# Kernel optimization log

Measured on AMD Instinct MI355X. Metric: run time of the kernel, lower is better.

The kernel has to match this reference:

```python
import jax, jax.numpy as jnp
import numpy as np

N_NODES = 50000
N_EDGES = 150000
N_GRAPHS = 1024
IN_DIM = 78
OUT_DIM = 64
HEADS = 10
HID = OUT_DIM * HEADS  # 640
NEG_SLOPE = 0.2


def _add_self_loops(edge_index, num_nodes):
    loop = jnp.arange(num_nodes, dtype=edge_index.dtype)
    src = jnp.concatenate([edge_index[0], loop])
    dst = jnp.concatenate([edge_index[1], loop])
    return src, dst


def gatv2_conv(x, edge_index, Wl, Wr, att, bias, heads, out_dim):
    # PyG GATv2Conv (share_weights=False, concat=True, add_self_loops=True),
    # inference mode so attention dropout is a no-op.
    N = x.shape[0]
    src, dst = _add_self_loops(edge_index, N)
    xl = (x @ Wl).reshape(N, heads, out_dim)  # source transform
    xr = (x @ Wr).reshape(N, heads, out_dim)  # target transform
    s = jax.nn.leaky_relu(xl[src] + xr[dst], NEG_SLOPE)      # [E,H,C]
    logits = jnp.einsum('ehc,hc->eh', s, att)                # [E,H]
    m = jax.ops.segment_max(logits, dst, num_segments=N)     # [N,H] (self-loops => no empty segs)
    ex = jnp.exp(logits - m[dst])
    den = jax.ops.segment_sum(ex, dst, num_segments=N)
    alpha = ex / den[dst]                                    # scatter-softmax over in-edges
    out = jax.ops.segment_sum(alpha[:, :, None] * xl[src], dst, num_segments=N)
    return out.reshape(N, heads * out_dim) + bias


def gcn_conv(x, edge_index, W, b):
    N = x.shape[0]
    src, dst = _add_self_loops(edge_index, N)
    deg = jax.ops.segment_sum(jnp.ones(src.shape[0], x.dtype), dst, num_segments=N)
    dinv = jax.lax.rsqrt(jnp.maximum(deg, 1.0))
    norm = dinv[src] * dinv[dst]                             # [E]
    xw = x @ W
    return jax.ops.segment_sum(norm[:, None] * xw[src], dst, num_segments=N) + b


def setup_inputs() -> dict:
    key = jax.random.key(0)
    ks = jax.random.split(key, 16)
    x = jax.random.normal(ks[0], (N_NODES, IN_DIM), dtype=jnp.float32)
    edge_index = jax.random.randint(ks[1], (2, N_EDGES), 0, N_NODES, dtype=jnp.int64)
    batch = jnp.sort(jax.random.randint(ks[2], (N_NODES,), 0, N_GRAPHS, dtype=jnp.int64))

    def glorot(k, shape, fan_in):
        return jax.random.normal(k, shape, dtype=jnp.float32) * (1.0 / np.sqrt(fan_in))

    return {
        'x': x, 'edge_index': edge_index, 'batch': batch,
        'Wl1': glorot(ks[3], (IN_DIM, HID), IN_DIM),
        'Wr1': glorot(ks[4], (IN_DIM, HID), IN_DIM),
        'a1': glorot(ks[5], (HEADS, OUT_DIM), OUT_DIM),
        'b1': jnp.zeros((HID,), jnp.float32),
        'Wl2': glorot(ks[6], (HID, HID), HID),
        'Wr2': glorot(ks[7], (HID, HID), HID),
        'a2': glorot(ks[8], (1, HID), HID),
        'b2': jnp.zeros((HID,), jnp.float32),
        'Wg': glorot(ks[9], (HID, HID), HID),
        'bg': jnp.zeros((HID,), jnp.float32),
    }


def reference(x, edge_index, batch, Wl1, Wr1, a1, b1, Wl2, Wr2, a2, b2, Wg, bg):
    # inference: feature dropout layers are identity
    h = jax.nn.elu(gatv2_conv(x, edge_index, Wl1, Wr1, a1, b1, HEADS, OUT_DIM))
    h = gatv2_conv(h, edge_index, Wl2, Wr2, a2, b2, 1, HID)
    h = gcn_conv(h, edge_index, Wg, bg)
    h = jax.nn.relu(h)
    # global max pool + global mean pool per graph
    gmax = jax.ops.segment_max(h, batch, num_segments=N_GRAPHS)
    cnt = jax.ops.segment_sum(jnp.ones((h.shape[0],), h.dtype), batch, num_segments=N_GRAPHS)
    gmean = jax.ops.segment_sum(h, batch, num_segments=N_GRAPHS) / jnp.maximum(cnt, 1.0)[:, None]
    return jnp.concatenate([gmax, gmean], axis=1)
```

## Files before the change

kernel.cpp:

```cpp
#include <hip/hip_runtime.h>
#include <hip/hip_bf16.h>
#include <cstdint>
#include <cstddef>

typedef __hip_bfloat16 bf16;

#define N_NODES  50000
#define N_EDGES  150000
#define E_TOT    (N_EDGES + N_NODES)
#define N_TILES  ((E_TOT + 15) / 16)
#define N_GRAPHS 1024
#define IN_DIM   78
#define K1P      128
#define OUT_DIM  64
#define HEADS    10
#define HID      640
#define NEG_SLOPE 0.2f
#define SCB      ((N_NODES + 255) / 256)

static __device__ __forceinline__ float b2f(bf16 v){ return __bfloat162float(v); }
static __device__ __forceinline__ bf16  f2b(float v){ return __float2bfloat16(v); }

__device__ __forceinline__ int clampi(int v, int hi){ return v < 0 ? 0 : (v >= hi ? hi - 1 : v); }

__device__ __forceinline__ float bf2f_bits(short s){
  return __uint_as_float(((unsigned)(unsigned short)s) << 16);
}
__device__ __forceinline__ short f2bf_bits(float v){
  unsigned u = __float_as_uint(v);
  return (short)((u + 0x7fffu + ((u >> 16) & 1u)) >> 16);
}
__device__ __forceinline__ short f2bf_trunc(float v){
  return (short)(__float_as_uint(v) >> 16);
}

__global__ __launch_bounds__(256) void fill_u32(unsigned* __restrict__ p, unsigned v, int n){
  int i = blockIdx.x * 256 + threadIdx.x;
  if (i < n) p[i] = v;
}

__global__ __launch_bounds__(256) void conv_x(const float* __restrict__ x, bf16* __restrict__ XB){
  int i = blockIdx.x * 256 + threadIdx.x;
  if (i >= N_NODES * K1P) return;
  int n = i / K1P, k = i - n * K1P;
  XB[i] = f2b(k < IN_DIM ? x[(size_t)n * IN_DIM + k] : 0.f);
}

__global__ __launch_bounds__(256) void conv_wT2(const float* __restrict__ W0,
                                                const float* __restrict__ W1,
                                                bf16* __restrict__ WT,
                                                int K, int N, int Kp){
  int i = blockIdx.x * 256 + threadIdx.x;
  const int per = N * Kp;
  if (i >= 2 * per) return;
  int m = i / per, r = i - m * per;
  const float* W = m == 0 ? W0 : W1;
  int n = r / Kp, k = r - n * Kp;
  WT[i] = f2b(k < K ? W[(size_t)k * N + n] : 0.f);
}

__global__ __launch_bounds__(256) void conv_wT3t(const float* __restrict__ W0,
                                                 const float* __restrict__ W1,
                                                 const float* __restrict__ W2,
                                                 bf16* __restrict__ WT){
  __shared__ float t[32][33];
  int m = blockIdx.z;
  const float* W = m == 0 ? W0 : (m == 1 ? W1 : W2);
  int n0 = blockIdx.x * 32, k0 = blockIdx.y * 32;
  int tx = threadIdx.x & 31, ty = threadIdx.x >> 5;
#pragma unroll
  for (int r = 0; r < 32; r += 8)
    t[ty + r][tx] = W[(size_t)(k0 + ty + r) * HID + n0 + tx];
  __syncthreads();
  bf16* O = WT + (size_t)m * HID * HID;
#pragma unroll
  for (int r = 0; r < 32; r += 8)
    O[(size_t)(n0 + ty + r) * HID + k0 + tx] = f2b(t[tx][ty + r]);
}

__global__ __launch_bounds__(256) void conv_attP(const float* __restrict__ a, bf16* __restrict__ P,
                                                 int heads){
  int i = blockIdx.x * 256 + threadIdx.x;
  if (i >= (HID / 32) * 512) return;
  int chunk = i >> 9;
  int lane  = (i >> 3) & 63;
  int j     = i & 7;
  int h = lane & 15;
  int k = (lane >> 4) * 8 + j;
  int c = chunk * 32 + k;
  float v = 0.f;
  if (heads == HEADS){ if (h < HEADS && (c >> 6) == h) v = a[c]; }
  else               { if (h == 0) v = a[c]; }
  P[i] = f2b(v);
}

#define BM 128
#define BN 128
#define BK 64

typedef __attribute__((ext_vector_type(8))) short bf16x8;
typedef __attribute__((ext_vector_type(4))) float f32x4;

typedef const __attribute__((address_space(1))) unsigned gu32;
typedef __attribute__((address_space(3))) unsigned lu32;

__global__ __launch_bounds__(256) void mfma_gemm(const bf16* __restrict__ A,
                                                 const bf16* __restrict__ BT,
                                                 bf16* __restrict__ C0,
                                                 bf16* __restrict__ C1,
                                                 int M, int Kp, int NB){
  int d   = blockIdx.x;
  int xcd = d & 7, j = d >> 3;
  int cb  = j % NB, ri = j / NB;
  int rb  = ri * 8 + xcd;
  const int row0 = rb * BM;
  if (row0 >= M) return;
  const int col0 = cb * BN;

  __shared__ short As[BM * BK];
  __shared__ short Bs[BN * BK];
  const int tid  = threadIdx.x;
  const int lane = tid & 63;
  const int wave = tid >> 6;
  const int wr   = (wave >> 1) * 64;
  const int wc   = (wave & 1) * 64;
  const int l15  = lane & 15;
  const int quad = lane >> 4;
  const int sw   = l15 & 7;

  const bf16* aptr[4];
  const bf16* bptr[4];
  lu32* lda[4];
  lu32* ldb[4];
#pragma unroll
  for (int t = 0; t < 4; ++t){
    int ci = (t * 4 + wave) * 64 + lane;
    int r  = ci >> 3;
    int sc = (ci & 7) ^ (r & 7);
    int gr = row0 + r; if (gr >= M) gr = M - 1;
    aptr[t] = A  + (size_t)gr * Kp + sc * 8;
    bptr[t] = BT + (size_t)(col0 + r) * Kp + sc * 8;
    lda[t]  = (lu32*)(&As[(t * 4 + wave) * 512]);
    ldb[t]  = (lu32*)(&Bs[(t * 4 + wave) * 512]);
  }

  f32x4 acc[4][4];
#pragma unroll
  for (int i = 0; i < 4; ++i)
#pragma unroll
    for (int jj = 0; jj < 4; ++jj) acc[i][jj] = (f32x4){0.f, 0.f, 0.f, 0.f};

  for (int k0 = 0; k0 < Kp; k0 += BK){
#pragma unroll
    for (int t = 0; t < 4; ++t){
      __builtin_amdgcn_global_load_lds((gu32*)(aptr[t] + k0), lda[t], 16, 0, 0);
      __builtin_amdgcn_global_load_lds((gu32*)(bptr[t] + k0), ldb[t], 16, 0, 0);
    }
    __syncthreads();

#pragma unroll
    for (int ks = 0; ks < 2; ++ks){
      const int slotA = ((ks * 4 + quad) ^ sw) * 8;
      bf16x8 af[4], bfr[4];
#pragma unroll
      for (int i = 0; i < 4; ++i)
        af[i] = *(bf16x8*)(&As[(wr + i * 16 + l15) * BK + slotA]);
#pragma unroll
      for (int jj = 0; jj < 4; ++jj)
        bfr[jj] = *(bf16x8*)(&Bs[(wc + jj * 16 + l15) * BK + slotA]);
#pragma unroll
      for (int i = 0; i < 4; ++i)
#pragma unroll
        for (int jj = 0; jj < 4; ++jj)
          acc[i][jj] = __builtin_amdgcn_mfma_f32_16x16x32_bf16(af[i], bfr[jj], acc[i][jj], 0, 0, 0);
    }
    __syncthreads();
  }

  if (row0 + BM <= M){
#pragma unroll
    for (int i = 0; i < 4; ++i){
#pragma unroll
      for (int jj = 0; jj < 4; ++jj){
        int gc = col0 + wc + jj * 16 + l15;
        bf16* Cp = (gc < HID) ? C0 : C1;
        size_t cc = (gc < HID) ? gc : gc - HID;
        size_t base = (size_t)(row0 + wr + i * 16 + quad * 4) * HID + cc;
#pragma unroll
        for (int r = 0; r < 4; ++r)
          Cp[base + (size_t)r * HID] = f2b(acc[i][jj][r]);
      }
    }
  } else {
#pragma unroll
    for (int i = 0; i < 4; ++i){
#pragma unroll
      for (int jj = 0; jj < 4; ++jj){
        int gc = col0 + wc + jj * 16 + l15;
        bf16* Cp = (gc < HID) ? C0 : C1;
        int cc   = (gc < HID) ? gc : gc - HID;
#pragma unroll
        for (int r = 0; r < 4; ++r){
          int gr = row0 + wr + i * 16 + quad * 4 + r;
          if (gr < M) Cp[(size_t)gr * HID + cc] = f2b(acc[i][jj][r]);
        }
      }
    }
  }
}

__global__ __launch_bounds__(256) void count_deg(const int* __restrict__ edst, int* __restrict__ degi){
  int e = blockIdx.x * 256 + threadIdx.x;
  if (e >= N_EDGES) return;
  atomicAdd(&degi[clampi(edst[e], N_NODES)], 1);
}

__global__ __launch_bounds__(256) void scan_blk(const int* __restrict__ degi,
                                                int* __restrict__ rowp,
                                                float* __restrict__ dinv,
                                                int* __restrict__ bsum){
  __shared__ int wsum[4];
  int b = blockIdx.x, tid = threadIdx.x;
  int i = b * 256 + tid;
  int lane = tid & 63, wv = tid >> 6;
  int v = (i < N_NODES) ? degi[i] : 0;
  int incl = v;
#pragma unroll
  for (int ofs = 1; ofs < 64; ofs <<= 1){
    int t = __shfl_up(incl, ofs);
    if (lane >= ofs) incl += t;
  }
  if (lane == 63) wsum[wv] = incl;
  __syncthreads();
  int woff = 0;
#pragma unroll
  for (int w = 0; w < 4; ++w) if (w < wv) woff += wsum[w];
  if (i < N_NODES){
    rowp[i] = woff + incl - v;
    dinv[i] = rsqrtf((float)(v + 1));
  }
  if (tid == 0) bsum[b] = wsum[0] + wsum[1] + wsum[2] + wsum[3];
}

__global__ __launch_bounds__(256) void scan_top(int* __restrict__ bsum, int* __restrict__ rowp){
  __shared__ int wsum[4];
  int tid = threadIdx.x, lane = tid & 63, wv = tid >> 6;
  int v = (tid < SCB) ? bsum[tid] : 0;
  int incl = v;
#pragma unroll
  for (int ofs = 1; ofs < 64; ofs <<= 1){
    int t = __shfl_up(incl, ofs);
    if (lane >= ofs) incl += t;
  }
  if (lane == 63) wsum[wv] = incl;
  __syncthreads();
  int woff = 0;
#pragma unroll
  for (int w = 0; w < 4; ++w) if (w < wv) woff += wsum[w];
  if (tid < SCB) bsum[tid] = woff + incl - v;
  if (tid == 255) rowp[N_NODES] = woff + incl;
}

__global__ __launch_bounds__(256) void scan_add(const int* __restrict__ bsum,
                                                int* __restrict__ rowp,
                                                int* __restrict__ curs){
  int i = blockIdx.x * 256 + threadIdx.x;
  if (i >= N_NODES) return;
  int r = rowp[i] + bsum[blockIdx.x];
  rowp[i] = r; curs[i] = r;
}

__global__ __launch_bounds__(256) void bucket_edges(const int* __restrict__ esrc,
                                                    const int* __restrict__ edst,
                                                    int* __restrict__ curs,
                                                    int* __restrict__ srcg,
                                                    int* __restrict__ dstg){
  int e = blockIdx.x * 256 + threadIdx.x;
  if (e >= N_EDGES) return;
  int d = clampi(edst[e], N_NODES);
  int pos = atomicAdd(&curs[d], 1);
  srcg[pos] = clampi(esrc[e], N_NODES);
  dstg[pos] = d;
}

__global__ __launch_bounds__(256) void logits_mfma(const bf16* __restrict__ xl,
                                                   const bf16* __restrict__ xr,
                                                   const int* __restrict__ srcg,
                                                   const int* __restrict__ dstg,
                                                   const bf16* __restrict__ attP,
                                                   float* __restrict__ LOG,
                                                   int only0){
  int wid  = (blockIdx.x * 256 + threadIdx.x) >> 6;
  int lane = threadIdx.x & 63;
  if (wid >= N_TILES) return;
  const int l15 = lane & 15, quad = lane >> 4;
  int p = wid * 16 + l15; if (p >= E_TOT) p = E_TOT - 1;
  int s, d;
  if (p < N_EDGES){ s = srcg[p]; d = dstg[p]; }
  else            { s = d = p - N_EDGES; }
  const bf16* ps = xl + (size_t)s * HID + quad * 8;
  const bf16* pd = xr + (size_t)d * HID + quad * 8;
  const bf16* pw = attP + lane * 8;

  f32x4 acc = (f32x4){0.f, 0.f, 0.f, 0.f};
  for (int k0 = 0; k0 < HID; k0 += 64){
    bf16x8 va0 = *(const bf16x8*)(ps + k0);
    bf16x8 vb0 = *(const bf16x8*)(pd + k0);
    bf16x8 va1 = *(const bf16x8*)(ps + k0 + 32);
    bf16x8 vb1 = *(const bf16x8*)(pd + k0 + 32);
    bf16x8 t0, t1;
#pragma unroll
    for (int j = 0; j < 8; ++j){
      float v0 = bf2f_bits(va0[j]) + bf2f_bits(vb0[j]);
      v0 *= (v0 > 0.f) ? 1.f : NEG_SLOPE;
      t0[j] = f2bf_trunc(v0);
      float v1 = bf2f_bits(va1[j]) + bf2f_bits(vb1[j]);
      v1 *= (v1 > 0.f) ? 1.f : NEG_SLOPE;
      t1[j] = f2bf_trunc(v1);
    }
    bf16x8 wb0 = *(const bf16x8*)(pw + (k0 >> 5) * 512);
    bf16x8 wb1 = *(const bf16x8*)(pw + ((k0 >> 5) + 1) * 512);
    acc = __builtin_amdgcn_mfma_f32_16x16x32_bf16(t0, wb0, acc, 0, 0, 0);
    acc = __builtin_amdgcn_mfma_f32_16x16x32_bf16(t1, wb1, acc, 0, 0, 0);
  }
  int er = wid * 16 + quad * 4;
  if (only0){
    if (l15 == 0){
#pragma unroll
      for (int r = 0; r < 4; ++r){
        int ee = er + r;
        if (ee < E_TOT) LOG[ee] = acc[r];
      }
    }
  } else {
#pragma unroll
    for (int r = 0; r < 4; ++r){
      int ee = er + r;
      if (ee < E_TOT) LOG[(size_t)ee * 16 + l15] = acc[r];
    }
  }
}

__global__ __launch_bounds__(256) void gat1_agg(const bf16* __restrict__ xl,
                                                const int* __restrict__ srcg,
                                                const int* __restrict__ rowp,
                                                const float* __restrict__ LOG,
                                                const float* __restrict__ bias,
                                                bf16* __restrict__ H){
  int n    = (blockIdx.x * 256 + threadIdx.x) >> 6;
  int lane = threadIdx.x & 63;
  if (n >= N_NODES) return;
  const int l15 = lane & 15;
  const int hA = lane >> 3;
  const int hB = 8 + (lane >> 5);
  int r0 = rowp[n], r1 = rowp[n + 1];

  float lself = LOG[(size_t)(N_EDGES + n) * 16 + l15];
  float m = lself;
  for (int p = r0; p < r1; ++p) m = fmaxf(m, LOG[(size_t)p * 16 + l15]);

  float p0  = __expf(lself - m);
  float den = p0;
  float accA[8], accB[2];
  {
    float pA = __shfl(p0, hA), pB = __shfl(p0, hB);
    const bf16* xn = xl + (size_t)n * HID;
    bf16x8 va = *(const bf16x8*)(xn + 8 * lane);
    unsigned vb = *(const unsigned*)(xn + 512 + 2 * lane);
#pragma unroll
    for (int j = 0; j < 8; ++j) accA[j] = pA * bf2f_bits(va[j]);
    accB[0] = pB * bf2f_bits((short)(vb & 0xffff));
    accB[1] = pB * bf2f_bits((short)(vb >> 16));
  }
  int p = r0;
  for (; p + 1 < r1; p += 2){
    int s0 = srcg[p], s1 = srcg[p + 1];
    float l0 = LOG[(size_t)p * 16 + l15];
    float l1 = LOG[(size_t)(p + 1) * 16 + l15];
    const bf16* xs0 = xl + (size_t)s0 * HID;
    const bf16* xs1 = xl + (size_t)s1 * HID;
    bf16x8 va0 = *(const bf16x8*)(xs0 + 8 * lane);
    bf16x8 va1 = *(const bf16x8*)(xs1 + 8 * lane);
    unsigned vb0 = *(const unsigned*)(xs0 + 512 + 2 * lane);
    unsigned vb1 = *(const unsigned*)(xs1 + 512 + 2 * lane);
    float pv0 = __expf(l0 - m), pv1 = __expf(l1 - m);
    den += pv0 + pv1;
    float pA0 = __shfl(pv0, hA), pB0 = __shfl(pv0, hB);
    float pA1 = __shfl(pv1, hA), pB1 = __shfl(pv1, hB);
#pragma unroll
    for (int j = 0; j < 8; ++j) accA[j] += pA0 * bf2f_bits(va0[j]) + pA1 * bf2f_bits(va1[j]);
    accB[0] += pB0 * bf2f_bits((short)(vb0 & 0xffff)) + pB1 * bf2f_bits((short)(vb1 & 0xffff));
    accB[1] += pB0 * bf2f_bits((short)(vb0 >> 16))    + pB1 * bf2f_bits((short)(vb1 >> 16));
  }
  if (p < r1){
    int s = srcg[p];
    float pv = __expf(LOG[(size_t)p * 16 + l15] - m);
    den += pv;
    float pA = __shfl(pv, hA), pB = __shfl(pv, hB);
    const bf16* xs = xl + (size_t)s * HID;
    bf16x8 va = *(const bf16x8*)(xs + 8 * lane);
    unsigned vb = *(const unsigned*)(xs + 512 + 2 * lane);
#pragma unroll
    for (int j = 0; j < 8; ++j) accA[j] += pA * bf2f_bits(va[j]);
    accB[0] += pB * bf2f_bits((short)(vb & 0xffff));
    accB[1] += pB * bf2f_bits((short)(vb >> 16));
  }
  float dA = __shfl(den, hA), dB = __shfl(den, hB);
  float4 bA0 = *(const float4*)(bias + 8 * lane);
  float4 bA1 = *(const float4*)(bias + 8 * lane + 4);
  float2 bB  = *(const float2*)(bias + 512 + 2 * lane);
  bf16x8 oA;
  float bAa[8] = {bA0.x, bA0.y, bA0.z, bA0.w, bA1.x, bA1.y, bA1.z, bA1.w};
#pragma unroll
  for (int j = 0; j < 8; ++j){
    float v = accA[j] / dA + bAa[j];
    v = v > 0.f ? v : (__expf(v) - 1.f);
    oA[j] = f2bf_bits(v);
  }
  float v0 = accB[0] / dB + bB.x; v0 = v0 > 0.f ? v0 : (__expf(v0) - 1.f);
  float v1 = accB[1] / dB + bB.y; v1 = v1 > 0.f ? v1 : (__expf(v1) - 1.f);
  bf16* hn = H + (size_t)n * HID;
  *(bf16x8*)(hn + 8 * lane) = oA;
  unsigned ob = (unsigned)(unsigned short)f2bf_bits(v0) |
                ((unsigned)(unsigned short)f2bf_bits(v1) << 16);
  *(unsigned*)(hn + 512 + 2 * lane) = ob;
}

__global__ __launch_bounds__(256) void gat2_agg(const bf16* __restrict__ xl,
                                                const int* __restrict__ srcg,
                                                const int* __restrict__ rowp,
                                                const float* __restrict__ LOG,
                                                const float* __restrict__ bias,
                                                bf16* __restrict__ H){
  int n    = (blockIdx.x * 256 + threadIdx.x) >> 6;
  int lane = threadIdx.x & 63;
  if (n >= N_NODES) return;
  int r0 = rowp[n], r1 = rowp[n + 1];

  float lself = LOG[N_EDGES + n];
  float m = lself;
  for (int p = r0; p < r1; ++p) m = fmaxf(m, LOG[p]);

  float p0  = __expf(lself - m);
  float den = p0;
  float accA[8], accB[2];
  {
    const bf16* xn = xl + (size_t)n * HID;
    bf16x8 va = *(const bf16x8*)(xn + 8 * lane);
    unsigned vb = *(const unsigned*)(xn + 512 + 2 * lane);
#pragma unroll
    for (int j = 0; j < 8; ++j) accA[j] = p0 * bf2f_bits(va[j]);
    accB[0] = p0 * bf2f_bits((short)(vb & 0xffff));
    accB[1] = p0 * bf2f_bits((short)(vb >> 16));
  }
  int p = r0;
  for (; p + 1 < r1; p += 2){
    int s0 = srcg[p], s1 = srcg[p + 1];
    float pv0 = __expf(LOG[p] - m), pv1 = __expf(LOG[p + 1] - m);
    const bf16* xs0 = xl + (size_t)s0 * HID;
    const bf16* xs1 = xl + (size_t)s1 * HID;
    bf16x8 va0 = *(const bf16x8*)(xs0 + 8 * lane);
    bf16x8 va1 = *(const bf16x8*)(xs1 + 8 * lane);
    unsigned vb0 = *(const unsigned*)(xs0 + 512 + 2 * lane);
    unsigned vb1 = *(const unsigned*)(xs1 + 512 + 2 * lane);
    den += pv0 + pv1;
#pragma unroll
    for (int j = 0; j < 8; ++j) accA[j] += pv0 * bf2f_bits(va0[j]) + pv1 * bf2f_bits(va1[j]);
    accB[0] += pv0 * bf2f_bits((short)(vb0 & 0xffff)) + pv1 * bf2f_bits((short)(vb1 & 0xffff));
    accB[1] += pv0 * bf2f_bits((short)(vb0 >> 16))    + pv1 * bf2f_bits((short)(vb1 >> 16));
  }
  if (p < r1){
    int s = srcg[p];
    float pv = __expf(LOG[p] - m);
    den += pv;
    const bf16* xs = xl + (size_t)s * HID;
    bf16x8 va = *(const bf16x8*)(xs + 8 * lane);
    unsigned vb = *(const unsigned*)(xs + 512 + 2 * lane);
#pragma unroll
    for (int j = 0; j < 8; ++j) accA[j] += pv * bf2f_bits(va[j]);
    accB[0] += pv * bf2f_bits((short)(vb & 0xffff));
    accB[1] += pv * bf2f_bits((short)(vb >> 16));
  }
  float inv = 1.f / den;
  float4 bA0 = *(const float4*)(bias + 8 * lane);
  float4 bA1 = *(const float4*)(bias + 8 * lane + 4);
  float2 bB  = *(const float2*)(bias + 512 + 2 * lane);
  float bAa[8] = {bA0.x, bA0.y, bA0.z, bA0.w, bA1.x, bA1.y, bA1.z, bA1.w};
  bf16x8 oA;
#pragma unroll
  for (int j = 0; j < 8; ++j) oA[j] = f2bf_bits(accA[j] * inv + bAa[j]);
  bf16* hn = H + (size_t)n * HID;
  *(bf16x8*)(hn + 8 * lane) = oA;
  unsigned ob = (unsigned)(unsigned short)f2bf_bits(accB[0] * inv + bB.x) |
                ((unsigned)(unsigned short)f2bf_bits(accB[1] * inv + bB.y) << 16);
  *(unsigned*)(hn + 512 + 2 * lane) = ob;
}

__global__ __launch_bounds__(256) void gcn_gather(const bf16* __restrict__ xw,
                                                  const int* __restrict__ srcg,
                                                  const int* __restrict__ rowp,
                                                  const float* __restrict__ dinv,
                                                  const float* __restrict__ bg,
                                                  bf16* __restrict__ h3){
  int n    = (blockIdx.x * 256 + threadIdx.x) >> 6;
  int lane = threadIdx.x & 63;
  if (n >= N_NODES) return;
  int r0 = rowp[n], r1 = rowp[n + 1];

  float dn = dinv[n];
  float accA[8], accB[2];
  {
    float w = dn * dn;
    const bf16* xn = xw + (size_t)n * HID;
    bf16x8 va = *(const bf16x8*)(xn + 8 * lane);
    unsigned vb = *(const unsigned*)(xn + 512 + 2 * lane);
#pragma unroll
    for (int j = 0; j < 8; ++j) accA[j] = w * bf2f_bits(va[j]);
    accB[0] = w * bf2f_bits((short)(vb & 0xffff));
    accB[1] = w * bf2f_bits((short)(vb >> 16));
  }
  int p = r0;
  for (; p + 1 < r1; p += 2){
    int s0 = srcg[p], s1 = srcg[p + 1];
    float w0 = dinv[s0] * dn, w1 = dinv[s1] * dn;
    const bf16* xs0 = xw + (size_t)s0 * HID;
    const bf16* xs1 = xw + (size_t)s1 * HID;
    bf16x8 va0 = *(const bf16x8*)(xs0 + 8 * lane);
    bf16x8 va1 = *(const bf16x8*)(xs1 + 8 * lane);
    unsigned vb0 = *(const unsigned*)(xs0 + 512 + 2 * lane);
    unsigned vb1 = *(const unsigned*)(xs1 + 512 + 2 * lane);
#pragma unroll
    for (int j = 0; j < 8; ++j) accA[j] += w0 * bf2f_bits(va0[j]) + w1 * bf2f_bits(va1[j]);
    accB[0] += w0 * bf2f_bits((short)(vb0 & 0xffff)) + w1 * bf2f_bits((short)(vb1 & 0xffff));
    accB[1] += w0 * bf2f_bits((short)(vb0 >> 16))    + w1 * bf2f_bits((short)(vb1 >> 16));
  }
  if (p < r1){
    int s = srcg[p];
    float w = dinv[s] * dn;
    const bf16* xs = xw + (size_t)s * HID;
    bf16x8 va = *(const bf16x8*)(xs + 8 * lane);
    unsigned vb = *(const unsigned*)(xs + 512 + 2 * lane);
#pragma unroll
    for (int j = 0; j < 8; ++j) accA[j] += w * bf2f_bits(va[j]);
    accB[0] += w * bf2f_bits((short)(vb & 0xffff));
    accB[1] += w * bf2f_bits((short)(vb >> 16));
  }
  float4 bA0 = *(const float4*)(bg + 8 * lane);
  float4 bA1 = *(const float4*)(bg + 8 * lane + 4);
  float2 bB  = *(const float2*)(bg + 512 + 2 * lane);
  float bAa[8] = {bA0.x, bA0.y, bA0.z, bA0.w, bA1.x, bA1.y, bA1.z, bA1.w};
  bf16x8 oA;
#pragma unroll
  for (int j = 0; j < 8; ++j) oA[j] = f2bf_bits(fmaxf(accA[j] + bAa[j], 0.f));
  bf16* hn = h3 + (size_t)n * HID;
  *(bf16x8*)(hn + 8 * lane) = oA;
  unsigned ob = (unsigned)(unsigned short)f2bf_bits(fmaxf(accB[0] + bB.x, 0.f)) |
                ((unsigned)(unsigned short)f2bf_bits(fmaxf(accB[1] + bB.y, 0.f)) << 16);
  *(unsigned*)(hn + 512 + 2 * lane) = ob;
}

__global__ __launch_bounds__(256) void graph_bounds(const int* __restrict__ batch,
                                                    int* __restrict__ gstart){
  int n = blockIdx.x * 256 + threadIdx.x;
  if (n >= N_NODES) return;
  int b = clampi(batch[n], N_GRAPHS);
  if (n == 0){
    for (int g = 0; g <= b; ++g) gstart[g] = 0;
  } else {
    int bp = clampi(batch[n - 1], N_GRAPHS);
    for (int g = bp + 1; g <= b; ++g) gstart[g] = n;
  }
  if (n == N_NODES - 1){
    for (int g = b + 1; g <= N_GRAPHS; ++g) gstart[g] = N_NODES;
  }
}

__global__ __launch_bounds__(640) void pool_graph(const bf16* __restrict__ h3,
                                                  const int* __restrict__ gstart,
                                                  float* __restrict__ out){
  int g = blockIdx.x;
  int c = threadIdx.x;
  int n0 = gstart[g], n1 = gstart[g + 1];
  float mx = 0.f, sm = 0.f;
  for (int n = n0; n < n1; ++n){
    float v = b2f(h3[(size_t)n * HID + c]);
    mx = fmaxf(mx, v); sm += v;
  }
  float mean = (n1 > n0) ? sm / (float)(n1 - n0) : 0.f;
  out[(size_t)g * 2 * HID + c]       = mx;
  out[(size_t)g * 2 * HID + HID + c] = mean;
}

extern "C" void kernel_launch(void* const* d_in, const int* in_sizes, int n_in,
                              void* d_out, int out_size, void* d_ws, size_t ws_size,
                              hipStream_t stream){
  const float* x     = (const float*)d_in[0];
  const int*   ei    = (const int*)d_in[1];
  const int*   batch = (const int*)d_in[2];
  const float* Wl1 = (const float*)d_in[3];
  const float* Wr1 = (const float*)d_in[4];
  const float* a1  = (const float*)d_in[5];
  const float* b1  = (const float*)d_in[6];
  const float* Wl2 = (const float*)d_in[7];
  const float* Wr2 = (const float*)d_in[8];
  const float* a2  = (const float*)d_in[9];
  const float* b2  = (const float*)d_in[10];
  const float* Wg  = (const float*)d_in[11];
  const float* bg  = (const float*)d_in[12];
  const int* esrc = ei;
  const int* edst = ei + N_EDGES;

  char* ws = (char*)d_ws;
  size_t off = 0;
  auto take = [&](size_t bytes)->char*{
    char* p = ws + off; off = (off + bytes + 255) & ~(size_t)255; return p;
  };
  bf16*     X1   = (bf16*)    take((size_t)N_NODES * HID * 2);
  bf16*     X2   = (bf16*)    take((size_t)N_NODES * HID * 2);
  bf16*     H    = (bf16*)    take((size_t)N_NODES * HID * 2);
  bf16*     XB   = (bf16*)    take((size_t)N_NODES * K1P * 2);
  bf16*     WT1l = (bf16*)    take((size_t)HID * K1P * 2);
  bf16*     WT1r = (bf16*)    take((size_t)HID * K1P * 2);
  bf16*     WT2l = (bf16*)    take((size_t)HID * HID * 2);
  bf16*     WT2r = (bf16*)    take((size_t)HID * HID * 2);
  bf16*     WTg  = (bf16*)    take((size_t)HID * HID * 2);
  bf16*     AT1P = (bf16*)    take((size_t)(HID / 32) * 512 * 2);
  bf16*     AT2P = (bf16*)    take((size_t)(HID / 32) * 512 * 2);
  float*    LOG  = (float*)   take((size_t)E_TOT * 16 * 4);
  int*      DEGI = (int*)     take((size_t)N_NODES * 4);
  int*      ROWP = (int*)     take((size_t)(N_NODES + 1) * 4);
  int*      CURS = (int*)     take((size_t)N_NODES * 4);
  int*      SRCG = (int*)     take((size_t)N_EDGES * 4);
  int*      DSTG = (int*)     take((size_t)N_EDGES * 4);
  float*    DINV = (float*)   take((size_t)N_NODES * 4);
  int*      GST  = (int*)     take((size_t)(N_GRAPHS + 1) * 4);
  int*      BSUM = (int*)     take((size_t)SCB * 4);

  dim3 blk(256);
  auto fill = [&](void* p, unsigned v, int n){
    fill_u32<<<dim3((n + 255) / 256), blk, 0, stream>>>((unsigned*)p, v, n);
  };
  const int MB8     = ((N_NODES + BM - 1) / BM + 7) / 8;
  const int nblocks = (N_NODES * 64 + 255) / 256;
  const int lblocks = (N_TILES * 64 + 255) / 256;
  const int reblk   = (N_EDGES + 255) / 256;
  const int apn     = (HID / 32) * 512;

  conv_x<<<(N_NODES * K1P + 255) / 256, blk, 0, stream>>>(x, XB);
  conv_wT2<<<(2 * HID * K1P + 255) / 256, blk, 0, stream>>>(Wl1, Wr1, WT1l, IN_DIM, HID, K1P);
  conv_wT3t<<<dim3(HID / 32, HID / 32, 3), blk, 0, stream>>>(Wl2, Wr2, Wg, WT2l);
  conv_attP<<<(apn + 255) / 256, blk, 0, stream>>>(a1, AT1P, HEADS);
  conv_attP<<<(apn + 255) / 256, blk, 0, stream>>>(a2, AT2P, 1);
  fill(DEGI, 0u, N_NODES);
  count_deg<<<reblk, blk, 0, stream>>>(edst, DEGI);
  scan_blk<<<dim3(SCB), blk, 0, stream>>>(DEGI, ROWP, DINV, BSUM);
  scan_top<<<dim3(1), blk, 0, stream>>>(BSUM, ROWP);
  scan_add<<<dim3(SCB), blk, 0, stream>>>(BSUM, ROWP, CURS);
  bucket_edges<<<reblk, blk, 0, stream>>>(esrc, edst, CURS, SRCG, DSTG);
  graph_bounds<<<(N_NODES + 255) / 256, blk, 0, stream>>>(batch, GST);

  mfma_gemm<<<dim3(8 * MB8 * 10), blk, 0, stream>>>(XB, WT1l, X1, X2, N_NODES, K1P, 10);
  logits_mfma<<<lblocks, blk, 0, stream>>>(X1, X2, SRCG, DSTG, AT1P, LOG, 0);
  gat1_agg<<<nblocks, blk, 0, stream>>>(X1, SRCG, ROWP, LOG, b1, H);

  mfma_gemm<<<dim3(8 * MB8 * 10), blk, 0, stream>>>(H, WT2l, X1, X2, N_NODES, HID, 10);
  logits_mfma<<<lblocks, blk, 0, stream>>>(X1, X2, SRCG, DSTG, AT2P, LOG, 1);
  gat2_agg<<<nblocks, blk, 0, stream>>>(X1, SRCG, ROWP, LOG, b2, H);

  mfma_gemm<<<dim3(8 * MB8 * 5), blk, 0, stream>>>(H, WTg, X1, X1, N_NODES, HID, 5);
  gcn_gather<<<nblocks, blk, 0, stream>>>(X1, SRCG, ROWP, DINV, bg, X2);
  pool_graph<<<dim3(N_GRAPHS), dim3(640), 0, stream>>>(X2, GST, (float*)d_out);
}
```

Measured before the change: 611.8 us.

## Fuse GATv2 logit computation into aggregation with online softmax

Removes the separate MFMA logits kernels and the edge-logit buffer, so each node's wavefront computes attention logits on the fly from the gathered source row and its own target row. It uses an online (running-max) softmax so the aggregation needs a single pass over in-edges. This avoids writing and re-reading a per-edge logit array and a second gather of source rows. In exchange it replaces MFMA dot products with scalar FMAs plus cross-lane shuffle reductions, and adds extra exp rescaling per edge pair.

```diff
diff --git a/kernel.cpp b/kernel.cpp
--- a/kernel.cpp
+++ b/kernel.cpp
@@ -7,8 +7,6 @@
 
 #define N_NODES  50000
 #define N_EDGES  150000
-#define E_TOT    (N_EDGES + N_NODES)
-#define N_TILES  ((E_TOT + 15) / 16)
 #define N_GRAPHS 1024
 #define IN_DIM   78
 #define K1P      128
@@ -29,9 +27,6 @@
 __device__ __forceinline__ short f2bf_bits(float v){
   unsigned u = __float_as_uint(v);
   return (short)((u + 0x7fffu + ((u >> 16) & 1u)) >> 16);
-}
-__device__ __forceinline__ short f2bf_trunc(float v){
-  return (short)(__float_as_uint(v) >> 16);
 }
 
 __global__ __launch_bounds__(256) void fill_u32(unsigned* __restrict__ p, unsigned v, int n){
@@ -76,22 +71,6 @@
 #pragma unroll
   for (int r = 0; r < 32; r += 8)
     O[(size_t)(n0 + ty + r) * HID + k0 + tx] = f2b(t[tx][ty + r]);
-}
-
-__global__ __launch_bounds__(256) void conv_attP(const float* __restrict__ a, bf16* __restrict__ P,
-                                                 int heads){
-  int i = blockIdx.x * 256 + threadIdx.x;
-  if (i >= (HID / 32) * 512) return;
-  int chunk = i >> 9;
-  int lane  = (i >> 3) & 63;
-  int j     = i & 7;
-  int h = lane & 15;
-  int k = (lane >> 4) * 8 + j;
-  int c = chunk * 32 + k;
-  float v = 0.f;
-  if (heads == HEADS){ if (h < HEADS && (c >> 6) == h) v = a[c]; }
-  else               { if (h == 0) v = a[c]; }
-  P[i] = f2b(v);
 }
 
 #define BM 128
@@ -283,204 +262,258 @@
   dstg[pos] = d;
 }
 
-__global__ __launch_bounds__(256) void logits_mfma(const bf16* __restrict__ xl,
-                                                   const bf16* __restrict__ xr,
-                                                   const int* __restrict__ srcg,
-                                                   const int* __restrict__ dstg,
-                                                   const bf16* __restrict__ attP,
-                                                   float* __restrict__ LOG,
-                                                   int only0){
-  int wid  = (blockIdx.x * 256 + threadIdx.x) >> 6;
-  int lane = threadIdx.x & 63;
-  if (wid >= N_TILES) return;
-  const int l15 = lane & 15, quad = lane >> 4;
-  int p = wid * 16 + l15; if (p >= E_TOT) p = E_TOT - 1;
-  int s, d;
-  if (p < N_EDGES){ s = srcg[p]; d = dstg[p]; }
-  else            { s = d = p - N_EDGES; }
-  const bf16* ps = xl + (size_t)s * HID + quad * 8;
-  const bf16* pd = xr + (size_t)d * HID + quad * 8;
-  const bf16* pw = attP + lane * 8;
-
-  f32x4 acc = (f32x4){0.f, 0.f, 0.f, 0.f};
-  for (int k0 = 0; k0 < HID; k0 += 64){
-    bf16x8 va0 = *(const bf16x8*)(ps + k0);
-    bf16x8 vb0 = *(const bf16x8*)(pd + k0);
-    bf16x8 va1 = *(const bf16x8*)(ps + k0 + 32);
-    bf16x8 vb1 = *(const bf16x8*)(pd + k0 + 32);
-    bf16x8 t0, t1;
-#pragma unroll
-    for (int j = 0; j < 8; ++j){
-      float v0 = bf2f_bits(va0[j]) + bf2f_bits(vb0[j]);
-      v0 *= (v0 > 0.f) ? 1.f : NEG_SLOPE;
-      t0[j] = f2bf_trunc(v0);
-      float v1 = bf2f_bits(va1[j]) + bf2f_bits(vb1[j]);
-      v1 *= (v1 > 0.f) ? 1.f : NEG_SLOPE;
-      t1[j] = f2bf_trunc(v1);
-    }
-    bf16x8 wb0 = *(const bf16x8*)(pw + (k0 >> 5) * 512);
-    bf16x8 wb1 = *(const bf16x8*)(pw + ((k0 >> 5) + 1) * 512);
-    acc = __builtin_amdgcn_mfma_f32_16x16x32_bf16(t0, wb0, acc, 0, 0, 0);
-    acc = __builtin_amdgcn_mfma_f32_16x16x32_bf16(t1, wb1, acc, 0, 0, 0);
-  }
-  int er = wid * 16 + quad * 4;
-  if (only0){
-    if (l15 == 0){
-#pragma unroll
-      for (int r = 0; r < 4; ++r){
-        int ee = er + r;
-        if (ee < E_TOT) LOG[ee] = acc[r];
-      }
-    }
-  } else {
-#pragma unroll
-    for (int r = 0; r < 4; ++r){
-      int ee = er + r;
-      if (ee < E_TOT) LOG[(size_t)ee * 16 + l15] = acc[r];
-    }
-  }
-}
-
-__global__ __launch_bounds__(256) void gat1_agg(const bf16* __restrict__ xl,
-                                                const int* __restrict__ srcg,
-                                                const int* __restrict__ rowp,
-                                                const float* __restrict__ LOG,
-                                                const float* __restrict__ bias,
-                                                bf16* __restrict__ H){
-  int n    = (blockIdx.x * 256 + threadIdx.x) >> 6;
-  int lane = threadIdx.x & 63;
-  if (n >= N_NODES) return;
-  const int l15 = lane & 15;
-  const int hA = lane >> 3;
-  const int hB = 8 + (lane >> 5);
-  int r0 = rowp[n], r1 = rowp[n + 1];
-
-  float lself = LOG[(size_t)(N_EDGES + n) * 16 + l15];
-  float m = lself;
-  for (int p = r0; p < r1; ++p) m = fmaxf(m, LOG[(size_t)p * 16 + l15]);
-
-  float p0  = __expf(lself - m);
-  float den = p0;
-  float accA[8], accB[2];
-  {
-    float pA = __shfl(p0, hA), pB = __shfl(p0, hB);
-    const bf16* xn = xl + (size_t)n * HID;
-    bf16x8 va = *(const bf16x8*)(xn + 8 * lane);
-    unsigned vb = *(const unsigned*)(xn + 512 + 2 * lane);
-#pragma unroll
-    for (int j = 0; j < 8; ++j) accA[j] = pA * bf2f_bits(va[j]);
-    accB[0] = pB * bf2f_bits((short)(vb & 0xffff));
-    accB[1] = pB * bf2f_bits((short)(vb >> 16));
-  }
-  int p = r0;
-  for (; p + 1 < r1; p += 2){
-    int s0 = srcg[p], s1 = srcg[p + 1];
-    float l0 = LOG[(size_t)p * 16 + l15];
-    float l1 = LOG[(size_t)(p + 1) * 16 + l15];
-    const bf16* xs0 = xl + (size_t)s0 * HID;
-    const bf16* xs1 = xl + (size_t)s1 * HID;
-    bf16x8 va0 = *(const bf16x8*)(xs0 + 8 * lane);
-    bf16x8 va1 = *(const bf16x8*)(xs1 + 8 * lane);
-    unsigned vb0 = *(const unsigned*)(xs0 + 512 + 2 * lane);
-    unsigned vb1 = *(const unsigned*)(xs1 + 512 + 2 * lane);
-    float pv0 = __expf(l0 - m), pv1 = __expf(l1 - m);
-    den += pv0 + pv1;
-    float pA0 = __shfl(pv0, hA), pB0 = __shfl(pv0, hB);
-    float pA1 = __shfl(pv1, hA), pB1 = __shfl(pv1, hB);
-#pragma unroll
-    for (int j = 0; j < 8; ++j) accA[j] += pA0 * bf2f_bits(va0[j]) + pA1 * bf2f_bits(va1[j]);
-    accB[0] += pB0 * bf2f_bits((short)(vb0 & 0xffff)) + pB1 * bf2f_bits((short)(vb1 & 0xffff));
-    accB[1] += pB0 * bf2f_bits((short)(vb0 >> 16))    + pB1 * bf2f_bits((short)(vb1 >> 16));
-  }
-  if (p < r1){
-    int s = srcg[p];
-    float pv = __expf(LOG[(size_t)p * 16 + l15] - m);
-    den += pv;
-    float pA = __shfl(pv, hA), pB = __shfl(pv, hB);
-    const bf16* xs = xl + (size_t)s * HID;
-    bf16x8 va = *(const bf16x8*)(xs + 8 * lane);
-    unsigned vb = *(const unsigned*)(xs + 512 + 2 * lane);
-#pragma unroll
-    for (int j = 0; j < 8; ++j) accA[j] += pA * bf2f_bits(va[j]);
-    accB[0] += pB * bf2f_bits((short)(vb & 0xffff));
-    accB[1] += pB * bf2f_bits((short)(vb >> 16));
-  }
-  float dA = __shfl(den, hA), dB = __shfl(den, hB);
-  float4 bA0 = *(const float4*)(bias + 8 * lane);
-  float4 bA1 = *(const float4*)(bias + 8 * lane + 4);
-  float2 bB  = *(const float2*)(bias + 512 + 2 * lane);
-  bf16x8 oA;
-  float bAa[8] = {bA0.x, bA0.y, bA0.z, bA0.w, bA1.x, bA1.y, bA1.z, bA1.w};
-#pragma unroll
-  for (int j = 0; j < 8; ++j){
-    float v = accA[j] / dA + bAa[j];
-    v = v > 0.f ? v : (__expf(v) - 1.f);
-    oA[j] = f2bf_bits(v);
-  }
-  float v0 = accB[0] / dB + bB.x; v0 = v0 > 0.f ? v0 : (__expf(v0) - 1.f);
-  float v1 = accB[1] / dB + bB.y; v1 = v1 > 0.f ? v1 : (__expf(v1) - 1.f);
-  bf16* hn = H + (size_t)n * HID;
-  *(bf16x8*)(hn + 8 * lane) = oA;
-  unsigned ob = (unsigned)(unsigned short)f2bf_bits(v0) |
-                ((unsigned)(unsigned short)f2bf_bits(v1) << 16);
-  *(unsigned*)(hn + 512 + 2 * lane) = ob;
-}
-
-__global__ __launch_bounds__(256) void gat2_agg(const bf16* __restrict__ xl,
-                                                const int* __restrict__ srcg,
-                                                const int* __restrict__ rowp,
-                                                const float* __restrict__ LOG,
-                                                const float* __restrict__ bias,
-                                                bf16* __restrict__ H){
+__global__ __launch_bounds__(256) void gat1_fused(const bf16* __restrict__ xl,
+                                                  const bf16* __restrict__ xr,
+                                                  const int* __restrict__ srcg,
+                                                  const int* __restrict__ rowp,
+                                                  const float* __restrict__ att,
+                                                  const float* __restrict__ bias,
+                                                  bf16* __restrict__ H){
   int n    = (blockIdx.x * 256 + threadIdx.x) >> 6;
   int lane = threadIdx.x & 63;
   if (n >= N_NODES) return;
   int r0 = rowp[n], r1 = rowp[n + 1];
 
-  float lself = LOG[N_EDGES + n];
-  float m = lself;
-  for (int p = r0; p < r1; ++p) m = fmaxf(m, LOG[p]);
-
-  float p0  = __expf(lself - m);
-  float den = p0;
-  float accA[8], accB[2];
-  {
-    const bf16* xn = xl + (size_t)n * HID;
-    bf16x8 va = *(const bf16x8*)(xn + 8 * lane);
-    unsigned vb = *(const unsigned*)(xn + 512 + 2 * lane);
-#pragma unroll
-    for (int j = 0; j < 8; ++j) accA[j] = p0 * bf2f_bits(va[j]);
-    accB[0] = p0 * bf2f_bits((short)(vb & 0xffff));
-    accB[1] = p0 * bf2f_bits((short)(vb >> 16));
-  }
+  float4 aA0 = *(const float4*)(att + 8 * lane);
+  float4 aA1 = *(const float4*)(att + 8 * lane + 4);
+  float2 aBv = *(const float2*)(att + 512 + 2 * lane);
+  float attA[8] = {aA0.x, aA0.y, aA0.z, aA0.w, aA1.x, aA1.y, aA1.z, aA1.w};
+  float attB0 = aBv.x, attB1 = aBv.y;
+
+  const bf16* xrn = xr + (size_t)n * HID;
+  bf16x8 vr = *(const bf16x8*)(xrn + 8 * lane);
+  unsigned ur = *(const unsigned*)(xrn + 512 + 2 * lane);
+  float xrA[8];
+#pragma unroll
+  for (int j = 0; j < 8; ++j) xrA[j] = bf2f_bits(vr[j]);
+  float xrB0 = bf2f_bits((short)(ur & 0xffff));
+  float xrB1 = bf2f_bits((short)(ur >> 16));
+
+  auto logits = [&](const float* xA, float xB0, float xB1, float& lA, float& lB){
+    float pa = 0.f;
+#pragma unroll
+    for (int j = 0; j < 8; ++j){
+      float s = xA[j] + xrA[j];
+      s *= (s > 0.f) ? 1.f : NEG_SLOPE;
+      pa = fmaf(attA[j], s, pa);
+    }
+    pa += __shfl_xor(pa, 1);
+    pa += __shfl_xor(pa, 2);
+    pa += __shfl_xor(pa, 4);
+    lA = pa;
+    float s0 = xB0 + xrB0; s0 *= (s0 > 0.f) ? 1.f : NEG_SLOPE;
+    float s1 = xB1 + xrB1; s1 *= (s1 > 0.f) ? 1.f : NEG_SLOPE;
+    float pb = attB0 * s0 + attB1 * s1;
+    pb += __shfl_xor(pb, 1);
+    pb += __shfl_xor(pb, 2);
+    pb += __shfl_xor(pb, 4);
+    pb += __shfl_xor(pb, 8);
+    pb += __shfl_xor(pb, 16);
+    lB = pb;
+  };
+
+  const bf16* xn = xl + (size_t)n * HID;
+  bf16x8 v0 = *(const bf16x8*)(xn + 8 * lane);
+  unsigned u0 = *(const unsigned*)(xn + 512 + 2 * lane);
+  float accA[8];
+  float sA[8];
+#pragma unroll
+  for (int j = 0; j < 8; ++j){ sA[j] = bf2f_bits(v0[j]); accA[j] = sA[j]; }
+  float sB0 = bf2f_bits((short)(u0 & 0xffff));
+  float sB1 = bf2f_bits((short)(u0 >> 16));
+  float accB0 = sB0, accB1 = sB1;
+  float mA, mB;
+  logits(sA, sB0, sB1, mA, mB);
+  float denA = 1.f, denB = 1.f;
+
   int p = r0;
   for (; p + 1 < r1; p += 2){
-    int s0 = srcg[p], s1 = srcg[p + 1];
-    float pv0 = __expf(LOG[p] - m), pv1 = __expf(LOG[p + 1] - m);
-    const bf16* xs0 = xl + (size_t)s0 * HID;
-    const bf16* xs1 = xl + (size_t)s1 * HID;
-    bf16x8 va0 = *(const bf16x8*)(xs0 + 8 * lane);
-    bf16x8 va1 = *(const bf16x8*)(xs1 + 8 * lane);
-    unsigned vb0 = *(const unsigned*)(xs0 + 512 + 2 * lane);
-    unsigned vb1 = *(const unsigned*)(xs1 + 512 + 2 * lane);
-    den += pv0 + pv1;
-#pragma unroll
-    for (int j = 0; j < 8; ++j) accA[j] += pv0 * bf2f_bits(va0[j]) + pv1 * bf2f_bits(va1[j]);
-    accB[0] += pv0 * bf2f_bits((short)(vb0 & 0xffff)) + pv1 * bf2f_bits((short)(vb1 & 0xffff));
-    accB[1] += pv0 * bf2f_bits((short)(vb0 >> 16))    + pv1 * bf2f_bits((short)(vb1 >> 16));
+    int s0i = srcg[p], s1i = srcg[p + 1];
+    const bf16* q0 = xl + (size_t)s0i * HID;
+    const bf16* q1 = xl + (size_t)s1i * HID;
+    bf16x8 w0 = *(const bf16x8*)(q0 + 8 * lane);
+    unsigned t0 = *(const unsigned*)(q0 + 512 + 2 * lane);
+    bf16x8 w1 = *(const bf16x8*)(q1 + 8 * lane);
+    unsigned t1 = *(const unsigned*)(q1 + 512 + 2 * lane);
+    float yA0[8], yA1[8];
+#pragma unroll
+    for (int j = 0; j < 8; ++j){ yA0[j] = bf2f_bits(w0[j]); yA1[j] = bf2f_bits(w1[j]); }
+    float yB00 = bf2f_bits((short)(t0 & 0xffff)), yB01 = bf2f_bits((short)(t0 >> 16));
+    float yB10 = bf2f_bits((short)(t1 & 0xffff)), yB11 = bf2f_bits((short)(t1 >> 16));
+    float lA0, lB0, lA1, lB1;
+    logits(yA0, yB00, yB01, lA0, lB0);
+    logits(yA1, yB10, yB11, lA1, lB1);
+    {
+      float m2 = fmaxf(mA, fmaxf(lA0, lA1));
+      float sc = __expf(mA - m2);
+      float p0 = __expf(lA0 - m2), p1 = __expf(lA1 - m2);
+      denA = denA * sc + p0 + p1; mA = m2;
+#pragma unroll
+      for (int j = 0; j < 8; ++j) accA[j] = accA[j] * sc + p0 * yA0[j] + p1 * yA1[j];
+    }
+    {
+      float m2 = fmaxf(mB, fmaxf(lB0, lB1));
+      float sc = __expf(mB - m2);
+      float p0 = __expf(lB0 - m2), p1 = __expf(lB1 - m2);
+      denB = denB * sc + p0 + p1; mB = m2;
+      accB0 = accB0 * sc + p0 * yB00 + p1 * yB10;
+      accB1 = accB1 * sc + p0 * yB01 + p1 * yB11;
+    }
   }
   if (p < r1){
-    int s = srcg[p];
-    float pv = __expf(LOG[p] - m);
-    den += pv;
-    const bf16* xs = xl + (size_t)s * HID;
-    bf16x8 va = *(const bf16x8*)(xs + 8 * lane);
-    unsigned vb = *(const unsigned*)(xs + 512 + 2 * lane);
-#pragma unroll
-    for (int j = 0; j < 8; ++j) accA[j] += pv * bf2f_bits(va[j]);
-    accB[0] += pv * bf2f_bits((short)(vb & 0xffff));
-    accB[1] += pv * bf2f_bits((short)(vb >> 16));
-  }
+    int si = srcg[p];
+    const bf16* q0 = xl + (size_t)si * HID;
+    bf16x8 w0 = *(const bf16x8*)(q0 + 8 * lane);
+    unsigned t0 = *(const unsigned*)(q0 + 512 + 2 * lane);
+    float yA0[8];
+#pragma unroll
+    for (int j = 0; j < 8; ++j) yA0[j] = bf2f_bits(w0[j]);
+    float yB00 = bf2f_bits((short)(t0 & 0xffff)), yB01 = bf2f_bits((short)(t0 >> 16));
+    float lA0, lB0;
+    logits(yA0, yB00, yB01, lA0, lB0);
+    {
+      float m2 = fmaxf(mA, lA0);
+      float sc = __expf(mA - m2);
+      float p0 = __expf(lA0 - m2);
+      denA = denA * sc + p0; mA = m2;
+#pragma unroll
+      for (int j = 0; j < 8; ++j) accA[j] = accA[j] * sc + p0 * yA0[j];
+    }
+    {
+      float m2 = fmaxf(mB, lB0);
+      float sc = __expf(mB - m2);
+      float p0 = __expf(lB0 - m2);
+      denB = denB * sc + p0; mB = m2;
+      accB0 = accB0 * sc + p0 * yB00;
+      accB1 = accB1 * sc + p0 * yB01;
+    }
+  }
+
+  float invA = 1.f / denA, invB = 1.f / denB;
+  float4 bA0 = *(const float4*)(bias + 8 * lane);
+  float4 bA1 = *(const float4*)(bias + 8 * lane + 4);
+  float2 bB  = *(const float2*)(bias + 512 + 2 * lane);
+  float bAa[8] = {bA0.x, bA0.y, bA0.z, bA0.w, bA1.x, bA1.y, bA1.z, bA1.w};
+  bf16x8 oA;
+#pragma unroll
+  for (int j = 0; j < 8; ++j){
+    float v = accA[j] * invA + bAa[j];
+    v = v > 0.f ? v : (__expf(v) - 1.f);
+    oA[j] = f2bf_bits(v);
+  }
+  float vb0 = accB0 * invB + bB.x; vb0 = vb0 > 0.f ? vb0 : (__expf(vb0) - 1.f);
+  float vb1 = accB1 * invB + bB.y; vb1 = vb1 > 0.f ? vb1 : (__expf(vb1) - 1.f);
+  bf16* hn = H + (size_t)n * HID;
+  *(bf16x8*)(hn + 8 * lane) = oA;
+  unsigned ob = (unsigned)(unsigned short)f2bf_bits(vb0) |
+                ((unsigned)(unsigned short)f2bf_bits(vb1) << 16);
+  *(unsigned*)(hn + 512 + 2 * lane) = ob;
+}
+
+__global__ __launch_bounds__(256) void gat2_fused(const bf16* __restrict__ xl,
+                                                  const bf16* __restrict__ xr,
+                                                  const int* __restrict__ srcg,
+                                                  const int* __restrict__ rowp,
+                                                  const float* __restrict__ att,
+                                                  const float* __restrict__ bias,
+                                                  bf16* __restrict__ H){
+  int n    = (blockIdx.x * 256 + threadIdx.x) >> 6;
+  int lane = threadIdx.x & 63;
+  if (n >= N_NODES) return;
+  int r0 = rowp[n], r1 = rowp[n + 1];
+
+  float4 aA0 = *(const float4*)(att + 8 * lane);
+  float4 aA1 = *(const float4*)(att + 8 * lane + 4);
+  float2 aBv = *(const float2*)(att + 512 + 2 * lane);
+  float attA[8] = {aA0.x, aA0.y, aA0.z, aA0.w, aA1.x, aA1.y, aA1.z, aA1.w};
+  float attB0 = aBv.x, attB1 = aBv.y;
+
+  const bf16* xrn = xr + (size_t)n * HID;
+  bf16x8 vr = *(const bf16x8*)(xrn + 8 * lane);
+  unsigned ur = *(const unsigned*)(xrn + 512 + 2 * lane);
+  float xrA[8];
+#pragma unroll
+  for (int j = 0; j < 8; ++j) xrA[j] = bf2f_bits(vr[j]);
+  float xrB0 = bf2f_bits((short)(ur & 0xffff));
+  float xrB1 = bf2f_bits((short)(ur >> 16));
+
+  auto logit1 = [&](const float* xA, float xB0, float xB1)->float{
+    float s0 = xB0 + xrB0; s0 *= (s0 > 0.f) ? 1.f : NEG_SLOPE;
+    float s1 = xB1 + xrB1; s1 *= (s1 > 0.f) ? 1.f : NEG_SLOPE;
+    float pa = attB0 * s0 + attB1 * s1;
+#pragma unroll
+    for (int j = 0; j < 8; ++j){
+      float s = xA[j] + xrA[j];
+      s *= (s > 0.f) ? 1.f : NEG_SLOPE;
+      pa = fmaf(attA[j], s, pa);
+    }
+    pa += __shfl_xor(pa, 1);
+    pa += __shfl_xor(pa, 2);
+    pa += __shfl_xor(pa, 4);
+    pa += __shfl_xor(pa, 8);
+    pa += __shfl_xor(pa, 16);
+    pa += __shfl_xor(pa, 32);
+    return pa;
+  };
+
+  const bf16* xn = xl + (size_t)n * HID;
+  bf16x8 v0 = *(const bf16x8*)(xn + 8 * lane);
+  unsigned u0 = *(const unsigned*)(xn + 512 + 2 * lane);
+  float accA[8];
+  float sA[8];
+#pragma unroll
+  for (int j = 0; j < 8; ++j){ sA[j] = bf2f_bits(v0[j]); accA[j] = sA[j]; }
+  float sB0 = bf2f_bits((short)(u0 & 0xffff));
+  float sB1 = bf2f_bits((short)(u0 >> 16));
+  float accB0 = sB0, accB1 = sB1;
+  float m = logit1(sA, sB0, sB1);
+  float den = 1.f;
+
+  int p = r0;
+  for (; p + 1 < r1; p += 2){
+    int s0i = srcg[p], s1i = srcg[p + 1];
+    const bf16* q0 = xl + (size_t)s0i * HID;
+    const bf16* q1 = xl + (size_t)s1i * HID;
+    bf16x8 w0 = *(const bf16x8*)(q0 + 8 * lane);
+    unsigned t0 = *(const unsigned*)(q0 + 512 + 2 * lane);
+    bf16x8 w1 = *(const bf16x8*)(q1 + 8 * lane);
+    unsigned t1 = *(const unsigned*)(q1 + 512 + 2 * lane);
+    float yA0[8], yA1[8];
+#pragma unroll
+    for (int j = 0; j < 8; ++j){ yA0[j] = bf2f_bits(w0[j]); yA1[j] = bf2f_bits(w1[j]); }
+    float yB00 = bf2f_bits((short)(t0 & 0xffff)), yB01 = bf2f_bits((short)(t0 >> 16));
+    float yB10 = bf2f_bits((short)(t1 & 0xffff)), yB11 = bf2f_bits((short)(t1 >> 16));
+    float l0 = logit1(yA0, yB00, yB01);
+    float l1 = logit1(yA1, yB10, yB11);
+    float m2 = fmaxf(m, fmaxf(l0, l1));
+    float sc = __expf(m - m2);
+    float p0 = __expf(l0 - m2), p1 = __expf(l1 - m2);
+    den = den * sc + p0 + p1; m = m2;
+#pragma unroll
+    for (int j = 0; j < 8; ++j) accA[j] = accA[j] * sc + p0 * yA0[j] + p1 * yA1[j];
+    accB0 = accB0 * sc + p0 * yB00 + p1 * yB10;
+    accB1 = accB1 * sc + p0 * yB01 + p1 * yB11;
+  }
+  if (p < r1){
+    int si = srcg[p];
+    const bf16* q0 = xl + (size_t)si * HID;
+    bf16x8 w0 = *(const bf16x8*)(q0 + 8 * lane);
+    unsigned t0 = *(const unsigned*)(q0 + 512 + 2 * lane);
+    float yA0[8];
+#pragma unroll
+    for (int j = 0; j < 8; ++j) yA0[j] = bf2f_bits(w0[j]);
+    float yB00 = bf2f_bits((short)(t0 & 0xffff)), yB01 = bf2f_bits((short)(t0 >> 16));
+    float l0 = logit1(yA0, yB00, yB01);
+    float m2 = fmaxf(m, l0);
+    float sc = __expf(m - m2);
+    float p0 = __expf(l0 - m2);
+    den = den * sc + p0; m = m2;
+#pragma unroll
+    for (int j = 0; j < 8; ++j) accA[j] = accA[j] * sc + p0 * yA0[j];
+    accB0 = accB0 * sc + p0 * yB00;
+    accB1 = accB1 * sc + p0 * yB01;
+  }
+
   float inv = 1.f / den;
   float4 bA0 = *(const float4*)(bias + 8 * lane);
   float4 bA1 = *(const float4*)(bias + 8 * lane + 4);
@@ -491,8 +524,8 @@
   for (int j = 0; j < 8; ++j) oA[j] = f2bf_bits(accA[j] * inv + bAa[j]);
   bf16* hn = H + (size_t)n * HID;
   *(bf16x8*)(hn + 8 * lane) = oA;
-  unsigned ob = (unsigned)(unsigned short)f2bf_bits(accB[0] * inv + bB.x) |
-                ((unsigned)(unsigned short)f2bf_bits(accB[1] * inv + bB.y) << 16);
+  unsigned ob = (unsigned)(unsigned short)f2bf_bits(accB0 * inv + bB.x) |
+                ((unsigned)(unsigned short)f2bf_bits(accB1 * inv + bB.y) << 16);
   *(unsigned*)(hn + 512 + 2 * lane) = ob;
 }
 
@@ -624,9 +657,6 @@
   bf16*     WT2l = (bf16*)    take((size_t)HID * HID * 2);
   bf16*     WT2r = (bf16*)    take((size_t)HID * HID * 2);
   bf16*     WTg  = (bf16*)    take((size_t)HID * HID * 2);
-  bf16*     AT1P = (bf16*)    take((size_t)(HID / 32) * 512 * 2);
-  bf16*     AT2P = (bf16*)    take((size_t)(HID / 32) * 512 * 2);
-  float*    LOG  = (float*)   take((size_t)E_TOT * 16 * 4);
   int*      DEGI = (int*)     take((size_t)N_NODES * 4);
   int*      ROWP = (int*)     take((size_t)(N_NODES + 1) * 4);
   int*      CURS = (int*)     take((size_t)N_NODES * 4);
@@ -635,6 +665,7 @@
   float*    DINV = (float*)   take((size_t)N_NODES * 4);
   int*      GST  = (int*)     take((size_t)(N_GRAPHS + 1) * 4);
   int*      BSUM = (int*)     take((size_t)SCB * 4);
+  (void)WT1r; (void)WT2r; (void)DSTG;
 
   dim3 blk(256);
   auto fill = [&](void* p, unsigned v, int n){
@@ -642,15 +673,11 @@
   };
   const int MB8     = ((N_NODES + BM - 1) / BM + 7) / 8;
   const int nblocks = (N_NODES * 64 + 255) / 256;
-  const int lblocks = (N_TILES * 64 + 255) / 256;
   const int reblk   = (N_EDGES + 255) / 256;
-  const int apn     = (HID / 32) * 512;
 
   conv_x<<<(N_NODES * K1P + 255) / 256, blk, 0, stream>>>(x, XB);
   conv_wT2<<<(2 * HID * K1P + 255) / 256, blk, 0, stream>>>(Wl1, Wr1, WT1l, IN_DIM, HID, K1P);
   conv_wT3t<<<dim3(HID / 32, HID / 32, 3), blk, 0, stream>>>(Wl2, Wr2, Wg, WT2l);
-  conv_attP<<<(apn + 255) / 256, blk, 0, stream>>>(a1, AT1P, HEADS);
-  conv_attP<<<(apn + 255) / 256, blk, 0, stream>>>(a2, AT2P, 1);
   fill(DEGI, 0u, N_NODES);
   count_deg<<<reblk, blk, 0, stream>>>(edst, DEGI);
   scan_blk<<<dim3(SCB), blk, 0, stream>>>(DEGI, ROWP, DINV, BSUM);
@@ -660,12 +687,10 @@
   graph_bounds<<<(N_NODES + 255) / 256, blk, 0, stream>>>(batch, GST);
 
   mfma_gemm<<<dim3(8 * MB8 * 10), blk, 0, stream>>>(XB, WT1l, X1, X2, N_NODES, K1P, 10);
-  logits_mfma<<<lblocks, blk, 0, stream>>>(X1, X2, SRCG, DSTG, AT1P, LOG, 0);
-  gat1_agg<<<nblocks, blk, 0, stream>>>(X1, SRCG, ROWP, LOG, b1, H);
+  gat1_fused<<<nblocks, blk, 0, stream>>>(X1, X2, SRCG, ROWP, a1, b1, H);
 
   mfma_gemm<<<dim3(8 * MB8 * 10), blk, 0, stream>>>(H, WT2l, X1, X2, N_NODES, HID, 10);
-  logits_mfma<<<lblocks, blk, 0, stream>>>(X1, X2, SRCG, DSTG, AT2P, LOG, 1);
-  gat2_agg<<<nblocks, blk, 0, stream>>>(X1, SRCG, ROWP, LOG, b2, H);
+  gat2_fused<<<nblocks, blk, 0, stream>>>(X1, X2, SRCG, ROWP, a2, b2, H);
 
   mfma_gemm<<<dim3(8 * MB8 * 5), blk, 0, stream>>>(H, WTg, X1, X1, N_NODES, HID, 5);
   gcn_gather<<<nblocks, blk, 0, stream>>>(X1, SRCG, ROWP, DINV, bg, X2);
```

New measurement: 511.5 us. 16.4% less time.
